# Kernel tuning notes

Hardware: AMD Instinct MI355X
Metric: run time of the kernel (lower is better)

Reference implementation:

```python
import jax, jax.numpy as jnp
import numpy as np

L, HID, NH, AD, FF = 6, 512, 8, 64, 2048
G, ST, NF, RA, RD = 8, 512, 25, 16, 20
T = G + 4 * ST  # 2056 tokens


def _ln(x, g, b, eps=1e-5):
    m = jnp.mean(x, axis=-1, keepdims=True)
    v = jnp.mean((x - m) ** 2, axis=-1, keepdims=True)
    return (x - m) * jax.lax.rsqrt(v + eps) * g + b


def _expand4(m, g):
    top = jnp.concatenate([m[:, :g, :g], jnp.repeat(m[:, :g, g:], 4, axis=2)], axis=2)
    bot = jnp.concatenate([jnp.repeat(m[:, g:, :g], 4, axis=1),
                           jnp.repeat(jnp.repeat(m[:, g:, g:], 4, axis=1), 4, axis=2)], axis=2)
    return jnp.concatenate([top, bot], axis=1)


def setup_inputs() -> dict:
    key = jax.random.key(0)
    ks = iter(jax.random.split(key, 48))
    n = lambda shape, s=0.02: (jax.random.normal(next(ks), shape, jnp.float32) * s)
    N = G + ST
    inp = {
        "obj_input": jax.random.normal(next(ks), (1, G, NF, 4), jnp.float32),
        "obj_scale": jax.random.normal(next(ks), (1, G, NF, 2), jnp.float32),
        "st_input0": jax.random.normal(next(ks), (1, ST, 10), jnp.float32),
        "rpe_a": jax.random.randint(next(ks), (1, N, N), 0, RA, jnp.int32),
        "rpe_d": jax.random.randint(next(ks), (1, N, N), 0, RD + 1, jnp.int32),
        "mask": jnp.zeros((1, N, N), jnp.float32),
        # projection heads
        "Wpg": n((4 * NF, HID)), "bpg": jnp.zeros((HID,)),
        "pg_g": jnp.ones((HID,)), "pg_b": jnp.zeros((HID,)),
        "Wps": n((2, HID)), "bps": jnp.zeros((HID,)),
        "ps_g": jnp.ones((HID,)), "ps_b": jnp.zeros((HID,)),
        # relative position embeddings
        "emb_a": n((RA, NH)), "emb_d": n((RD + 1, NH)),
        # stacked transformer layer params
        "Wq": n((L, HID, NH * AD)), "bq": jnp.zeros((L, NH * AD)),
        "Wk": n((L, HID, NH * AD)), "bk": jnp.zeros((L, NH * AD)),
        "Wv": n((L, HID, NH * AD)), "bv": jnp.zeros((L, NH * AD)),
        "Wo": n((L, NH * AD, HID)), "bo": jnp.zeros((L, HID)),
        "W1": n((L, HID, FF)), "b1": jnp.zeros((L, FF)),
        "W2": n((L, FF, HID)), "b2": jnp.zeros((L, HID)),
        "ln1_g": jnp.ones((L, HID)), "ln1_b": jnp.zeros((L, HID)),
        "ln2_g": jnp.ones((L, HID)), "ln2_b": jnp.zeros((L, HID)),
    }
    return inp


def reference(obj_input, obj_scale, st_input0, rpe_a, rpe_d, mask,
              Wpg, bpg, pg_g, pg_b, Wps, bps, ps_g, ps_b, emb_a, emb_d,
              Wq, bq, Wk, bk, Wv, bv, Wo, bo, W1, b1, W2, b2,
              ln1_g, ln1_b, ln2_g, ln2_b):
    g = obj_input.shape[1]
    # token embeddings: objects + strokes (4 points of 2 coords each)
    st = st_input0[:, :, :8].reshape(1, -1, 2)                       # [1, 4*ST, 2]
    obj_emb = jax.nn.leaky_relu(_ln(obj_input.reshape(1, g, -1) @ Wpg + bpg, pg_g, pg_b))
    st_emb = jax.nn.leaky_relu(_ln(st @ Wps + bps, ps_g, ps_b))
    x = jnp.concatenate([obj_emb, st_emb], axis=1)                   # [1, T, HID]
    t = x.shape[1]
    # relative-position bias: embed expanded angle/distance indices
    pos = emb_a[_expand4(rpe_a, g)] + emb_d[_expand4(rpe_d, g)]      # [1, T, T, NH]
    pos = jnp.transpose(pos, (0, 3, 1, 2))                           # [1, NH, T, T]
    msk = _expand4(mask, g)[:, None]                                 # [1, 1, T, T]
    inv_sqrt_d = np.float32(1.0 / np.sqrt(AD))
    for l in range(Wq.shape[0]):
        q = (x @ Wq[l] + bq[l]).reshape(1, t, NH, AD)
        k = (x @ Wk[l] + bk[l]).reshape(1, t, NH, AD)
        v = (x @ Wv[l] + bv[l]).reshape(1, t, NH, AD)
        # note: bias added BEFORE scaling, then mask (matches torch source)
        scores = (jnp.einsum('bqhd,bkhd->bhqk', q, k) + pos) * inv_sqrt_d + msk
        att = jax.nn.softmax(scores, axis=-1)
        o = jnp.einsum('bhqk,bkhd->bqhd', att, v).reshape(1, t, NH * AD)
        x = _ln(x + o @ Wo[l] + bo[l], ln1_g[l], ln1_b[l])
        h = jax.nn.leaky_relu(x @ W1[l] + b1[l])
        x = _ln(x + h @ W2[l] + b2[l], ln2_g[l], ln2_b[l])
    return x
```

## Files before the change

kernel.cpp:

```cpp
#include <hip/hip_runtime.h>
#include <math.h>

#define T_TOK 2056
#define TP 2176
#define TK 2112
#define HIDDEN 512
#define NHEAD 8
#define ADIM 64
#define FFDIM 2048
#define NLAYER 6
#define NORIG 520
#define NOBJ 8
#define NSPLIT 4

typedef float f32x4 __attribute__((ext_vector_type(4)));
typedef __attribute__((__ext_vector_type__(8))) __bf16 bf16x8;

__device__ __forceinline__ unsigned short f2bf(float f) {
  unsigned int u = __float_as_uint(f);
  u += 0x7FFFu + ((u >> 16) & 1u);
  return (unsigned short)(u >> 16);
}
__device__ __forceinline__ float bf2f(unsigned short u) {
  return __uint_as_float(((unsigned int)u) << 16);
}


__device__ inline float blockReduceSum(float v, float* sb) {
#pragma unroll
  for (int off = 32; off > 0; off >>= 1) v += __shfl_down(v, off, 64);
  int wid = threadIdx.x >> 6;
  __syncthreads();
  if ((threadIdx.x & 63) == 0) sb[wid] = v;
  __syncthreads();
  return sb[0] + sb[1] + sb[2] + sb[3];
}


__global__ __launch_bounds__(256) void embed_kernel(
    const float* __restrict__ obj, const float* __restrict__ st0,
    const float* __restrict__ Wpg, const float* __restrict__ bpg,
    const float* __restrict__ pg_g, const float* __restrict__ pg_b,
    const float* __restrict__ Wps, const float* __restrict__ bps,
    const float* __restrict__ ps_g, const float* __restrict__ ps_b,
    float* __restrict__ x, unsigned short* __restrict__ xb)
{
  __shared__ float sb[4];
  int t = blockIdx.x;
  int j0 = threadIdx.x, j1 = threadIdx.x + 256;
  float a0, a1;
  const float *g, *b;
  if (t < NOBJ) {
    a0 = bpg[j0]; a1 = bpg[j1];
    const float* in = obj + t * 100;
    for (int i = 0; i < 100; i++) {
      float w = in[i];
      a0 += w * Wpg[i * HIDDEN + j0];
      a1 += w * Wpg[i * HIDDEN + j1];
    }
    g = pg_g; b = pg_b;
  } else {
    int tt = t - NOBJ, s = tt >> 2, p = tt & 3;
    float c0 = st0[s * 10 + p * 2], c1 = st0[s * 10 + p * 2 + 1];
    a0 = bps[j0] + c0 * Wps[j0] + c1 * Wps[HIDDEN + j0];
    a1 = bps[j1] + c0 * Wps[j1] + c1 * Wps[HIDDEN + j1];
    g = ps_g; b = ps_b;
  }
  float s1 = blockReduceSum(a0 + a1, sb);
  float s2 = blockReduceSum(a0 * a0 + a1 * a1, sb);
  float m = s1 * (1.0f / HIDDEN);
  float var = s2 * (1.0f / HIDDEN) - m * m;
  float inv = rsqrtf(var + 1e-5f);
  float y0 = (a0 - m) * inv * g[j0] + b[j0];
  float y1 = (a1 - m) * inv * g[j1] + b[j1];
  y0 = y0 >= 0.f ? y0 : 0.01f * y0;
  y1 = y1 >= 0.f ? y1 : 0.01f * y1;
  x[t * HIDDEN + j0] = y0;
  x[t * HIDDEN + j1] = y1;
  xb[t * HIDDEN + j0] = f2bf(y0);
  xb[t * HIDDEN + j1] = f2bf(y1);
}

__global__ __launch_bounds__(256) void padzero(unsigned short* __restrict__ xb) {
  int i = blockIdx.x * 256 + threadIdx.x;
  if (i < (TP - T_TOK) * HIDDEN) xb[T_TOK * HIDDEN + i] = 0;
}


__global__ __launch_bounds__(256) void posbuild(
    const int* __restrict__ rpe_a, const int* __restrict__ rpe_d,
    const float* __restrict__ emb_a, const float* __restrict__ emb_d,
    const float* __restrict__ mask, unsigned short* __restrict__ posb)
{
  int i = blockIdx.x;
  for (int j = threadIdx.x; j < NORIG; j += 256) {
    int a = rpe_a[i * NORIG + j];
    int d = rpe_d[i * NORIG + j];
    float mk = mask[i * NORIG + j];
#pragma unroll
    for (int h = 0; h < NHEAD; h++) {
      float v = (emb_a[a * NHEAD + h] + emb_d[d * NHEAD + h]) * 0.125f + mk;
      posb[(h * NORIG + i) * NORIG + j] = f2bf(v);
    }
  }
}


__global__ __launch_bounds__(256) void wtrans(
    const float* __restrict__ Wq, const float* __restrict__ Wk, const float* __restrict__ Wv,
    const float* __restrict__ Wo, const float* __restrict__ W1, const float* __restrict__ W2,
    unsigned short* __restrict__ Wqkvt, unsigned short* __restrict__ Wot,
    unsigned short* __restrict__ W1t, unsigned short* __restrict__ W2t)
{
  __shared__ float t[64 * 65];
  int b = blockIdx.x;
  const float* src; unsigned short* dst; int N, K, tk, tn;
  if (b < 192) {
    int m = b >> 6, bb = b & 63;
    src = m == 0 ? Wq : m == 1 ? Wk : Wv;
    dst = Wqkvt + m * 512 * 512;
    K = 512; N = 512; tk = bb & 7; tn = bb >> 3;
  } else if (b < 256) {
    int bb = b - 192; src = Wo; dst = Wot; K = 512; N = 512; tk = bb & 7; tn = bb >> 3;
  } else if (b < 512) {
    int bb = b - 256; src = W1; dst = W1t; K = 512; N = 2048; tk = bb & 7; tn = bb >> 3;
  } else {
    int bb = b - 512; src = W2; dst = W2t; K = 2048; N = 512; tk = bb & 31; tn = bb >> 5;
  }
  int k0 = tk * 64, n0 = tn * 64;
  int tid = threadIdx.x;
  int r = tid >> 2, c0 = (tid & 3) * 16;
  const float* sp = src + (k0 + r) * N + n0 + c0;
#pragma unroll
  for (int q = 0; q < 4; q++) {
    float4 f = *(const float4*)(sp + q * 4);
    t[r * 65 + c0 + q * 4 + 0] = f.x;
    t[r * 65 + c0 + q * 4 + 1] = f.y;
    t[r * 65 + c0 + q * 4 + 2] = f.z;
    t[r * 65 + c0 + q * 4 + 3] = f.w;
  }
  __syncthreads();
  unsigned short vals[16];
#pragma unroll
  for (int j = 0; j < 16; j++) vals[j] = f2bf(t[(c0 + j) * 65 + r]);
  unsigned short* dp = dst + (n0 + r) * K + k0 + c0;
  *(int4*)dp = *(int4*)&vals[0];
  *(int4*)(dp + 8) = *(int4*)&vals[8];
}


__global__ __launch_bounds__(256) void gemm_bt(
    const unsigned short* __restrict__ A, int lda,
    const unsigned short* __restrict__ Bt, int ldb, int K, int mode,
    const float* __restrict__ b0, const float* __restrict__ b1, const float* __restrict__ b2,
    unsigned short* __restrict__ d0, unsigned short* __restrict__ d1, unsigned short* __restrict__ d2,
    float* __restrict__ df, int ldc)
{
  __shared__ unsigned short As[64 * 40];
  __shared__ unsigned short Bs[128 * 40];
  const int tid = threadIdx.x;
  const int lane = tid & 63, wave = tid >> 6;
  const int l15 = lane & 15, quad = lane >> 4;
  const int rowBase = blockIdx.y * 64, colBase = blockIdx.x * 128;
  const int mw = (wave & 1) * 32, nw = (wave >> 1) * 64;
  const int sr = tid >> 2, sc = (tid & 3) * 8;
  const int zz = blockIdx.z;
  const int kLen = K / gridDim.z;
  const int kb0 = zz * kLen;
  const unsigned short* Ag0 = A + (rowBase + sr) * lda + sc;
  const unsigned short* Bg0 = Bt + (colBase + sr) * ldb + sc;
  const unsigned short* Bg1 = Bg0 + 64 * ldb;
  f32x4 acc[2][4];
#pragma unroll
  for (int i = 0; i < 2; i++)
#pragma unroll
    for (int j = 0; j < 4; j++) acc[i][j] = (f32x4){0.f, 0.f, 0.f, 0.f};

  for (int kb = kb0; kb < kb0 + kLen; kb += 32) {
    int4 a0 = *(const int4*)(Ag0 + kb);
    int4 g0 = *(const int4*)(Bg0 + kb);
    int4 g1 = *(const int4*)(Bg1 + kb);
    __syncthreads();
    *(int4*)&As[sr * 40 + sc] = a0;
    *(int4*)&Bs[sr * 40 + sc] = g0;
    *(int4*)&Bs[(sr + 64) * 40 + sc] = g1;
    __syncthreads();
    bf16x8 af[2], bfr[4];
#pragma unroll
    for (int mt = 0; mt < 2; mt++)
      af[mt] = *(const bf16x8*)&As[(mw + mt * 16 + l15) * 40 + quad * 8];
#pragma unroll
    for (int nt = 0; nt < 4; nt++)
      bfr[nt] = *(const bf16x8*)&Bs[(nw + nt * 16 + l15) * 40 + quad * 8];
#pragma unroll
    for (int mt = 0; mt < 2; mt++)
#pragma unroll
      for (int nt = 0; nt < 4; nt++)
        acc[mt][nt] = __builtin_amdgcn_mfma_f32_16x16x32_bf16(af[mt], bfr[nt], acc[mt][nt], 0, 0, 0);
  }

  float* dfz = df + (size_t)zz * TP * ldc;
#pragma unroll
  for (int mt = 0; mt < 2; mt++) {
#pragma unroll
    for (int nt = 0; nt < 4; nt++) {
#pragma unroll
      for (int r = 0; r < 4; r++) {
        int row = rowBase + mw + mt * 16 + quad * 4 + r;
        int col = colBase + nw + nt * 16 + l15;
        float v = acc[mt][nt][r];
        if (mode == 0) {
          int seg = col >> 9, cc = col & 511;
          const float* bs = seg == 0 ? b0 : seg == 1 ? b1 : b2;
          unsigned short* dst = seg == 0 ? d0 : seg == 1 ? d1 : d2;
          int hd = cc >> 6, d = cc & 63;
          dst[(hd * TP + row) * 64 + d] = f2bf(v + bs[cc]);
        } else if (mode == 1) {
          dfz[row * ldc + col] = v;
        } else {
          float t = v + b0[col];
          t = t >= 0.f ? t : 0.01f * t;
          d0[row * ldc + col] = f2bf(t);
        }
      }
    }
  }
}


__global__ __launch_bounds__(256) void vt_trans(
    const unsigned short* __restrict__ vh, unsigned short* __restrict__ vt)
{
  __shared__ unsigned short t[64 * 72];
  int kt = blockIdx.x, h = blockIdx.y;
  int tid = threadIdx.x;
  int r0 = tid >> 3, cs = (tid & 7) * 8;
  const unsigned short* src = vh + (h * TP + kt * 64 + r0) * 64 + cs;
  *(int4*)&t[r0 * 72 + cs] = *(const int4*)src;
  *(int4*)&t[(r0 + 32) * 72 + cs] = *(const int4*)(src + 32 * 64);
  __syncthreads();
  int d = tid >> 2, c0 = (tid & 3) * 16;
  unsigned short vals[16];
#pragma unroll
  for (int j = 0; j < 16; j++) vals[j] = t[(c0 + j) * 72 + d];
  unsigned short* dst = vt + (h * 64 + d) * TK + kt * 64 + c0;
  *(int4*)dst = *(int4*)&vals[0];
  *(int4*)(dst + 8) = *(int4*)&vals[8];
}


__global__ __launch_bounds__(256) void flash_attn(
    const unsigned short* __restrict__ qh, const unsigned short* __restrict__ kh,
    const unsigned short* __restrict__ vt, const unsigned short* __restrict__ posb,
    float* __restrict__ Opart, float* __restrict__ ml)
{
  __shared__ unsigned short Ks[64 * 72];
  __shared__ unsigned short Vs[80 * 88];
  __shared__ unsigned short Ps[64 * 72];
  __shared__ float pt[24 * 24];
  const int tid = threadIdx.x;
  const int lane = tid & 63, wave = tid >> 6;
  const int l15 = lane & 15, quad = lane >> 4;
  const int qt = blockIdx.x, h = blockIdx.y, z = blockIdx.z;
  const int q0 = qt * 64;
  const int qrow = q0 + wave * 16 + l15;
  const unsigned short* qbp = qh + (h * TP + qrow) * 64;
  bf16x8 qf0 = *(const bf16x8*)(qbp + quad * 8);
  bf16x8 qf1 = *(const bf16x8*)(qbp + 32 + quad * 8);
  f32x4 O[5];
#pragma unroll
  for (int nt = 0; nt < 5; nt++) O[nt] = (f32x4){0.f, 0.f, 0.f, 0.f};
  for (int idx = tid; idx < 16 * 88; idx += 256) {
    int rr = idx / 88, cc = idx - rr * 88;
    Vs[(64 + rr) * 88 + cc] = (rr == 0) ? 0x3F80 : 0;
  }
  const int oq0 = q0 < 8 ? q0 : 8 + ((q0 - 8) >> 2);
  const int qe = min(q0 + 63, T_TOK - 1);
  const int nq = (qe < 8 ? qe : 8 + ((qe - 8) >> 2)) - oq0 + 1;
  int myq[4];
#pragma unroll
  for (int r = 0; r < 4; r++) {
    int qr = q0 + wave * 16 + quad * 4 + r;
    myq[r] = (qr < 8 ? qr : 8 + ((qr - 8) >> 2)) - oq0;
  }
  const int sr = tid >> 3, sc = (tid & 7) * 8;
  const unsigned short* kgb = kh + (h * TP + sr) * 64 + sc;
  const unsigned short* vgb = vt + (h * 64 + sr) * TK + sc;
  const int ptrow = tid >> 3, ptc0 = (tid & 7) * 3;

  const int kt0 = z * 9, kt1 = min(33, kt0 + 9);
  for (int kt = kt0; kt < kt1; kt++) {
    const int kb = kt * 64;
    int4 kv0 = *(const int4*)(kgb + kb * 64);
    int4 kv1 = *(const int4*)(kgb + (kb + 32) * 64);
    int4 vv0 = *(const int4*)(vgb + kb);
    int4 vv1 = *(const int4*)(vgb + 32 * TK + kb);
    const int ok0 = kb < 8 ? kb : 8 + ((kb - 8) >> 2);
    const int ke = min(kb + 63, T_TOK - 1);
    const int nk = (ke < 8 ? ke : 8 + ((ke - 8) >> 2)) - ok0 + 1;
    __syncthreads();
    *(int4*)&Ks[sr * 72 + sc] = kv0;
    *(int4*)&Ks[(sr + 32) * 72 + sc] = kv1;
    *(int4*)&Vs[sr * 88 + sc] = vv0;
    *(int4*)&Vs[(sr + 32) * 88 + sc] = vv1;
    if (ptrow < 24) {
      const unsigned short* prow = posb + (h * NORIG + oq0 + ptrow) * NORIG + ok0;
      bool rok = ptrow < nq;
#pragma unroll
      for (int c = 0; c < 3; c++) {
        int col = ptc0 + c;
        pt[ptrow * 24 + col] = (rok && col < nk) ? bf2f(prow[col]) : 0.f;
      }
    }
    __syncthreads();
    f32x4 S[4];
#pragma unroll
    for (int nt = 0; nt < 4; nt++) S[nt] = (f32x4){0.f, 0.f, 0.f, 0.f};
#pragma unroll
    for (int nt = 0; nt < 4; nt++) {
      bf16x8 kf0 = *(const bf16x8*)&Ks[(nt * 16 + l15) * 72 + quad * 8];
      bf16x8 kf1 = *(const bf16x8*)&Ks[(nt * 16 + l15) * 72 + 32 + quad * 8];
      S[nt] = __builtin_amdgcn_mfma_f32_16x16x32_bf16(qf0, kf0, S[nt], 0, 0, 0);
      S[nt] = __builtin_amdgcn_mfma_f32_16x16x32_bf16(qf1, kf1, S[nt], 0, 0, 0);
    }
    int okp[4], colv[4];
#pragma unroll
    for (int nt = 0; nt < 4; nt++) {
      int c = kb + nt * 16 + l15;
      colv[nt] = c;
      okp[nt] = (c < 8 ? c : 8 + ((c - 8) >> 2)) - ok0;
    }
#pragma unroll
    for (int r = 0; r < 4; r++) {
      int pr = wave * 16 + quad * 4 + r;
#pragma unroll
      for (int nt = 0; nt < 4; nt++) {
        float a = (colv[nt] < T_TOK)
                    ? fminf(S[nt][r] * 0.125f + pt[myq[r] * 24 + okp[nt]], 60.f)
                    : -1e30f;
        Ps[pr * 72 + nt * 16 + l15] = f2bf(__expf(a));
      }
    }
    __syncthreads();
    bf16x8 pa0 = *(const bf16x8*)&Ps[(wave * 16 + l15) * 72 + quad * 8];
    bf16x8 pa1 = *(const bf16x8*)&Ps[(wave * 16 + l15) * 72 + 32 + quad * 8];
#pragma unroll
    for (int nt = 0; nt < 5; nt++) {
      bf16x8 vb0 = *(const bf16x8*)&Vs[(nt * 16 + l15) * 88 + quad * 8];
      bf16x8 vb1 = *(const bf16x8*)&Vs[(nt * 16 + l15) * 88 + 32 + quad * 8];
      O[nt] = __builtin_amdgcn_mfma_f32_16x16x32_bf16(pa0, vb0, O[nt], 0, 0, 0);
      O[nt] = __builtin_amdgcn_mfma_f32_16x16x32_bf16(pa1, vb1, O[nt], 0, 0, 0);
    }
  }
#pragma unroll
  for (int r = 0; r < 4; r++) {
    float lsum = __shfl(O[4][r], lane & 48, 64);
    int orow = q0 + wave * 16 + quad * 4 + r;
    size_t base = ((size_t)(z * NHEAD + h) * TK + orow);
    if (l15 == 0) {
      ml[base * 2] = 0.f;
      ml[base * 2 + 1] = lsum;
    }
#pragma unroll
    for (int nt = 0; nt < 4; nt++)
      Opart[base * 64 + nt * 16 + l15] = O[nt][r];
  }
}


__global__ __launch_bounds__(256) void flash_merge(
    const float* __restrict__ Opart, const float* __restrict__ ml,
    unsigned short* __restrict__ ob)
{
  int idx = blockIdx.x * 256 + threadIdx.x;
  if (idx >= T_TOK * HIDDEN) return;
  int row = idx >> 9, c = idx & 511;
  int h = c >> 6, d = c & 63;
  float M = -1e30f;
  float mv[NSPLIT], lv[NSPLIT];
#pragma unroll
  for (int s = 0; s < NSPLIT; s++) {
    size_t base = ((size_t)(s * NHEAD + h) * TK + row);
    mv[s] = ml[base * 2];
    lv[s] = ml[base * 2 + 1];
    M = fmaxf(M, mv[s]);
  }
  float num = 0.f, den = 0.f;
#pragma unroll
  for (int s = 0; s < NSPLIT; s++) {
    float w = __expf(mv[s] - M);
    den += w * lv[s];
    num += w * Opart[((size_t)(s * NHEAD + h) * TK + row) * 64 + d];
  }
  ob[idx] = f2bf(num / den);
}


__global__ __launch_bounds__(256) void ln_residual4(
    float* __restrict__ x, const float* __restrict__ parts,
    const float* __restrict__ bias,
    const float* __restrict__ g, const float* __restrict__ b,
    unsigned short* __restrict__ xb)
{
  __shared__ float sb[4];
  int row = blockIdx.x;
  int j0 = threadIdx.x, j1 = threadIdx.x + 256;
  int base = row * HIDDEN;
  const size_t ss = (size_t)TP * HIDDEN;
  float v0 = x[base + j0] + bias[j0] + parts[base + j0] + parts[ss + base + j0]
           + parts[2 * ss + base + j0] + parts[3 * ss + base + j0];
  float v1 = x[base + j1] + bias[j1] + parts[base + j1] + parts[ss + base + j1]
           + parts[2 * ss + base + j1] + parts[3 * ss + base + j1];
  float s1 = blockReduceSum(v0 + v1, sb);
  float s2 = blockReduceSum(v0 * v0 + v1 * v1, sb);
  float m = s1 * (1.0f / HIDDEN);
  float var = s2 * (1.0f / HIDDEN) - m * m;
  float inv = rsqrtf(var + 1e-5f);
  float y0 = (v0 - m) * inv * g[j0] + b[j0];
  float y1 = (v1 - m) * inv * g[j1] + b[j1];
  x[base + j0] = y0;
  x[base + j1] = y1;
  xb[base + j0] = f2bf(y0);
  xb[base + j1] = f2bf(y1);
}

__global__ __launch_bounds__(256) void copy_out(
    const float4* __restrict__ src, float4* __restrict__ dst, int n4)
{
  int i = blockIdx.x * 256 + threadIdx.x;
  if (i < n4) dst[i] = src[i];
}


extern "C" void kernel_launch(void* const* d_in, const int* in_sizes, int n_in,
                              void* d_out, int out_size, void* d_ws, size_t ws_size,
                              hipStream_t stream) {
  const float* obj   = (const float*)d_in[0];
  const float* st0   = (const float*)d_in[2];
  const int*   rpe_a = (const int*)d_in[3];
  const int*   rpe_d = (const int*)d_in[4];
  const float* mask  = (const float*)d_in[5];
  const float* Wpg = (const float*)d_in[6];  const float* bpg = (const float*)d_in[7];
  const float* pg_g = (const float*)d_in[8]; const float* pg_b = (const float*)d_in[9];
  const float* Wps = (const float*)d_in[10]; const float* bps = (const float*)d_in[11];
  const float* ps_g = (const float*)d_in[12];const float* ps_b = (const float*)d_in[13];
  const float* emb_a = (const float*)d_in[14];
  const float* emb_d = (const float*)d_in[15];
  const float* Wq = (const float*)d_in[16]; const float* bq = (const float*)d_in[17];
  const float* Wk = (const float*)d_in[18]; const float* bk = (const float*)d_in[19];
  const float* Wv = (const float*)d_in[20]; const float* bv = (const float*)d_in[21];
  const float* Wo = (const float*)d_in[22]; const float* bo = (const float*)d_in[23];
  const float* W1 = (const float*)d_in[24]; const float* b1 = (const float*)d_in[25];
  const float* W2 = (const float*)d_in[26]; const float* b2 = (const float*)d_in[27];
  const float* ln1_g = (const float*)d_in[28]; const float* ln1_b = (const float*)d_in[29];
  const float* ln2_g = (const float*)d_in[30]; const float* ln2_b = (const float*)d_in[31];

  char* p = (char*)d_ws;
  auto alloc = [&](size_t bytes) { char* q = p; p += (bytes + 255) & ~(size_t)255; return q; };
  float*          x      = (float*)alloc((size_t)T_TOK * HIDDEN * 4);
  unsigned short* xb     = (unsigned short*)alloc((size_t)TP * HIDDEN * 2);
  char*           u1     = (char*)alloc((size_t)TP * FFDIM * 2);
  unsigned short* qhb    = (unsigned short*)u1;
  unsigned short* khb    = qhb + (size_t)NHEAD * TP * ADIM;
  unsigned short* vhb    = khb + (size_t)NHEAD * TP * ADIM;
  unsigned short* vtb    = vhb + (size_t)NHEAD * TP * ADIM;
  unsigned short* hb     = (unsigned short*)u1;
  unsigned short* ob     = (unsigned short*)alloc((size_t)TP * HIDDEN * 2);
  char*           u2     = (char*)alloc((size_t)NSPLIT * NHEAD * TK * ADIM * 4 + (size_t)NSPLIT * NHEAD * TK * 2 * 4);
  float*          Opart  = (float*)u2;
  float*          mlb    = Opart + (size_t)NSPLIT * NHEAD * TK * ADIM;
  float*          parts  = (float*)u2;
  unsigned short* posb   = (unsigned short*)alloc((size_t)NHEAD * NORIG * NORIG * 2);
  unsigned short* Wqkvt  = (unsigned short*)alloc((size_t)1536 * 512 * 2);
  unsigned short* Wot    = (unsigned short*)alloc((size_t)512 * 512 * 2);
  unsigned short* W1t    = (unsigned short*)alloc((size_t)2048 * 512 * 2);
  unsigned short* W2t    = (unsigned short*)alloc((size_t)512 * 2048 * 2);
  if ((size_t)(p - (char*)d_ws) > ws_size) return;

  float* out = (float*)d_out;

  embed_kernel<<<T_TOK, 256, 0, stream>>>(obj, st0, Wpg, bpg, pg_g, pg_b,
                                          Wps, bps, ps_g, ps_b, x, xb);
  padzero<<<((TP - T_TOK) * HIDDEN + 255) / 256, 256, 0, stream>>>(xb);
  posbuild<<<NORIG, 256, 0, stream>>>(rpe_a, rpe_d, emb_a, emb_d, mask, posb);

  for (int l = 0; l < NLAYER; l++) {
    wtrans<<<768, 256, 0, stream>>>(
        Wq + l * 512 * 512, Wk + l * 512 * 512, Wv + l * 512 * 512,
        Wo + l * 512 * 512, W1 + l * 512 * 2048, W2 + l * 2048 * 512,
        Wqkvt, Wot, W1t, W2t);
    gemm_bt<<<dim3(12, 34, 1), 256, 0, stream>>>(
        xb, HIDDEN, Wqkvt, HIDDEN, HIDDEN, 0,
        bq + l * 512, bk + l * 512, bv + l * 512, qhb, khb, vhb, nullptr, 0);
    vt_trans<<<dim3(33, 8), 256, 0, stream>>>(vhb, vtb);
    flash_attn<<<dim3(33, 8, NSPLIT), 256, 0, stream>>>(
        qhb, khb, vtb, posb, Opart, mlb);
    flash_merge<<<(T_TOK * HIDDEN + 255) / 256, 256, 0, stream>>>(Opart, mlb, ob);
    gemm_bt<<<dim3(4, 34, NSPLIT), 256, 0, stream>>>(
        ob, HIDDEN, Wot, HIDDEN, HIDDEN, 1,
        nullptr, nullptr, nullptr, nullptr, nullptr, nullptr, parts, HIDDEN);
    ln_residual4<<<T_TOK, 256, 0, stream>>>(x, parts, bo + l * 512,
                                            ln1_g + l * 512, ln1_b + l * 512, xb);
    gemm_bt<<<dim3(16, 34, 1), 256, 0, stream>>>(
        xb, HIDDEN, W1t, HIDDEN, HIDDEN, 2,
        b1 + l * 2048, nullptr, nullptr, hb, nullptr, nullptr, nullptr, FFDIM);
    gemm_bt<<<dim3(4, 34, NSPLIT), 256, 0, stream>>>(
        hb, FFDIM, W2t, FFDIM, FFDIM, 1,
        nullptr, nullptr, nullptr, nullptr, nullptr, nullptr, parts, HIDDEN);
    ln_residual4<<<T_TOK, 256, 0, stream>>>(x, parts, b2 + l * 512,
                                            ln2_g + l * 512, ln2_b + l * 512, xb);
  }

  int n4 = T_TOK * HIDDEN / 4;
  copy_out<<<(n4 + 255) / 256, 256, 0, stream>>>((const float4*)x, (float4*)out, n4);
}
```

Before: 1.004 ms.

## Double-buffer GEMM, prefetch flash tiles, use exp2 with prescaled Q, hoist weight transposes

The GEMM main loop now uses double-buffered LDS with register prefetch of the next K slice, which removes one barrier per iteration. The attention kernel splits keys 8 ways in an interleaved order and prefetches the next K/V/pos tile. It folds the 1/sqrt(d) scale and log2(e) into Q and the position bias so exp2 can be used, stores partial outputs as bf16, and drops one barrier. The merge becomes a plain sum, because no running max is kept. Weight transposes for all layers are done once up front when workspace allows, which adds memory use and relies on the clamp at 86 to avoid overflow.

```diff
diff --git a/kernel.cpp b/kernel.cpp
--- a/kernel.cpp
+++ b/kernel.cpp
@@ -12,9 +12,16 @@
 #define NORIG 520
 #define NOBJ 8
 #define NSPLIT 4
+#define FSPLIT 8
 
 typedef float f32x4 __attribute__((ext_vector_type(4)));
 typedef __attribute__((__ext_vector_type__(8))) __bf16 bf16x8;
+
+#if __has_builtin(__builtin_amdgcn_exp2f)
+#define EXP2(x) __builtin_amdgcn_exp2f(x)
+#else
+#define EXP2(x) exp2f(x)
+#endif
 
 __device__ __forceinline__ unsigned short f2bf(float f) {
   unsigned int u = __float_as_uint(f);
@@ -99,7 +106,7 @@
     float mk = mask[i * NORIG + j];
 #pragma unroll
     for (int h = 0; h < NHEAD; h++) {
-      float v = (emb_a[a * NHEAD + h] + emb_d[d * NHEAD + h]) * 0.125f + mk;
+      float v = ((emb_a[a * NHEAD + h] + emb_d[d * NHEAD + h]) * 0.125f + mk) * 1.44269504f;
       posb[(h * NORIG + i) * NORIG + j] = f2bf(v);
     }
   }
@@ -156,8 +163,8 @@
     unsigned short* __restrict__ d0, unsigned short* __restrict__ d1, unsigned short* __restrict__ d2,
     float* __restrict__ df, int ldc)
 {
-  __shared__ unsigned short As[64 * 40];
-  __shared__ unsigned short Bs[128 * 40];
+  __shared__ unsigned short As[2][64 * 40];
+  __shared__ unsigned short Bs[2][128 * 40];
   const int tid = threadIdx.x;
   const int lane = tid & 63, wave = tid >> 6;
   const int l15 = lane & 15, quad = lane >> 4;
@@ -167,6 +174,7 @@
   const int zz = blockIdx.z;
   const int kLen = K / gridDim.z;
   const int kb0 = zz * kLen;
+  const int nIter = kLen >> 5;
   const unsigned short* Ag0 = A + (rowBase + sr) * lda + sc;
   const unsigned short* Bg0 = Bt + (colBase + sr) * ldb + sc;
   const unsigned short* Bg1 = Bg0 + 64 * ldb;
@@ -176,27 +184,40 @@
 #pragma unroll
     for (int j = 0; j < 4; j++) acc[i][j] = (f32x4){0.f, 0.f, 0.f, 0.f};
 
-  for (int kb = kb0; kb < kb0 + kLen; kb += 32) {
-    int4 a0 = *(const int4*)(Ag0 + kb);
-    int4 g0 = *(const int4*)(Bg0 + kb);
-    int4 g1 = *(const int4*)(Bg1 + kb);
+  int4 a0 = *(const int4*)(Ag0 + kb0);
+  int4 g0 = *(const int4*)(Bg0 + kb0);
+  int4 g1 = *(const int4*)(Bg1 + kb0);
+  *(int4*)&As[0][sr * 40 + sc] = a0;
+  *(int4*)&Bs[0][sr * 40 + sc] = g0;
+  *(int4*)&Bs[0][(sr + 64) * 40 + sc] = g1;
+
+  for (int it = 0; it < nIter; ++it) {
     __syncthreads();
-    *(int4*)&As[sr * 40 + sc] = a0;
-    *(int4*)&Bs[sr * 40 + sc] = g0;
-    *(int4*)&Bs[(sr + 64) * 40 + sc] = g1;
-    __syncthreads();
+    const int cur = it & 1, nxt = cur ^ 1;
+    const bool more = (it + 1) < nIter;
+    if (more) {
+      int kb = kb0 + (it + 1) * 32;
+      a0 = *(const int4*)(Ag0 + kb);
+      g0 = *(const int4*)(Bg0 + kb);
+      g1 = *(const int4*)(Bg1 + kb);
+    }
     bf16x8 af[2], bfr[4];
 #pragma unroll
     for (int mt = 0; mt < 2; mt++)
-      af[mt] = *(const bf16x8*)&As[(mw + mt * 16 + l15) * 40 + quad * 8];
+      af[mt] = *(const bf16x8*)&As[cur][(mw + mt * 16 + l15) * 40 + quad * 8];
 #pragma unroll
     for (int nt = 0; nt < 4; nt++)
-      bfr[nt] = *(const bf16x8*)&Bs[(nw + nt * 16 + l15) * 40 + quad * 8];
+      bfr[nt] = *(const bf16x8*)&Bs[cur][(nw + nt * 16 + l15) * 40 + quad * 8];
 #pragma unroll
     for (int mt = 0; mt < 2; mt++)
 #pragma unroll
       for (int nt = 0; nt < 4; nt++)
         acc[mt][nt] = __builtin_amdgcn_mfma_f32_16x16x32_bf16(af[mt], bfr[nt], acc[mt][nt], 0, 0, 0);
+    if (more) {
+      *(int4*)&As[nxt][sr * 40 + sc] = a0;
+      *(int4*)&Bs[nxt][sr * 40 + sc] = g0;
+      *(int4*)&Bs[nxt][(sr + 64) * 40 + sc] = g1;
+    }
   }
 
   float* dfz = df + (size_t)zz * TP * ldc;
@@ -214,7 +235,9 @@
           const float* bs = seg == 0 ? b0 : seg == 1 ? b1 : b2;
           unsigned short* dst = seg == 0 ? d0 : seg == 1 ? d1 : d2;
           int hd = cc >> 6, d = cc & 63;
-          dst[(hd * TP + row) * 64 + d] = f2bf(v + bs[cc]);
+          float t = v + bs[cc];
+          if (seg == 0) t *= 0.180336880111f;
+          dst[(hd * TP + row) * 64 + d] = f2bf(t);
         } else if (mode == 1) {
           dfz[row * ldc + col] = v;
         } else {
@@ -252,7 +275,7 @@
 __global__ __launch_bounds__(256) void flash_attn(
     const unsigned short* __restrict__ qh, const unsigned short* __restrict__ kh,
     const unsigned short* __restrict__ vt, const unsigned short* __restrict__ posb,
-    float* __restrict__ Opart, float* __restrict__ ml)
+    unsigned short* __restrict__ Opart, float* __restrict__ lbuf)
 {
   __shared__ unsigned short Ks[64 * 72];
   __shared__ unsigned short Vs[80 * 88];
@@ -287,32 +310,53 @@
   const unsigned short* kgb = kh + (h * TP + sr) * 64 + sc;
   const unsigned short* vgb = vt + (h * 64 + sr) * TK + sc;
   const int ptrow = tid >> 3, ptc0 = (tid & 7) * 3;
-
-  const int kt0 = z * 9, kt1 = min(33, kt0 + 9);
-  for (int kt = kt0; kt < kt1; kt++) {
-    const int kb = kt * 64;
-    int4 kv0 = *(const int4*)(kgb + kb * 64);
-    int4 kv1 = *(const int4*)(kgb + (kb + 32) * 64);
-    int4 vv0 = *(const int4*)(vgb + kb);
-    int4 vv1 = *(const int4*)(vgb + 32 * TK + kb);
-    const int ok0 = kb < 8 ? kb : 8 + ((kb - 8) >> 2);
-    const int ke = min(kb + 63, T_TOK - 1);
-    const int nk = (ke < 8 ? ke : 8 + ((ke - 8) >> 2)) - ok0 + 1;
+  const bool prok = (ptrow < 24) && (ptrow < nq);
+
+  const int nT = (33 - z + FSPLIT - 1) / FSPLIT;
+  int kb = z * 64;
+  int4 kv0 = *(const int4*)(kgb + kb * 64);
+  int4 kv1 = *(const int4*)(kgb + (kb + 32) * 64);
+  int4 vv0 = *(const int4*)(vgb + kb);
+  int4 vv1 = *(const int4*)(vgb + 32 * TK + kb);
+  float ppf0, ppf1, ppf2;
+  {
+    int ok0n = kb < 8 ? kb : 8 + ((kb - 8) >> 2);
+    int ken = min(kb + 63, T_TOK - 1);
+    int nkn = (ken < 8 ? ken : 8 + ((ken - 8) >> 2)) - ok0n + 1;
+    const unsigned short* prow = posb + (h * NORIG + oq0 + ptrow) * NORIG + ok0n;
+    ppf0 = (prok && ptc0 + 0 < nkn) ? bf2f(prow[ptc0 + 0]) : 0.f;
+    ppf1 = (prok && ptc0 + 1 < nkn) ? bf2f(prow[ptc0 + 1]) : 0.f;
+    ppf2 = (prok && ptc0 + 2 < nkn) ? bf2f(prow[ptc0 + 2]) : 0.f;
+  }
+
+  for (int i = 0; i < nT; ++i) {
+    const int kbCur = kb;
+    const int ok0c = kbCur < 8 ? kbCur : 8 + ((kbCur - 8) >> 2);
     __syncthreads();
     *(int4*)&Ks[sr * 72 + sc] = kv0;
     *(int4*)&Ks[(sr + 32) * 72 + sc] = kv1;
     *(int4*)&Vs[sr * 88 + sc] = vv0;
     *(int4*)&Vs[(sr + 32) * 88 + sc] = vv1;
     if (ptrow < 24) {
-      const unsigned short* prow = posb + (h * NORIG + oq0 + ptrow) * NORIG + ok0;
-      bool rok = ptrow < nq;
-#pragma unroll
-      for (int c = 0; c < 3; c++) {
-        int col = ptc0 + c;
-        pt[ptrow * 24 + col] = (rok && col < nk) ? bf2f(prow[col]) : 0.f;
-      }
+      pt[ptrow * 24 + ptc0 + 0] = ppf0;
+      pt[ptrow * 24 + ptc0 + 1] = ppf1;
+      pt[ptrow * 24 + ptc0 + 2] = ppf2;
     }
     __syncthreads();
+    kb += FSPLIT * 64;
+    if (i + 1 < nT) {
+      kv0 = *(const int4*)(kgb + kb * 64);
+      kv1 = *(const int4*)(kgb + (kb + 32) * 64);
+      vv0 = *(const int4*)(vgb + kb);
+      vv1 = *(const int4*)(vgb + 32 * TK + kb);
+      int ok0n = kb < 8 ? kb : 8 + ((kb - 8) >> 2);
+      int ken = min(kb + 63, T_TOK - 1);
+      int nkn = (ken < 8 ? ken : 8 + ((ken - 8) >> 2)) - ok0n + 1;
+      const unsigned short* prow = posb + (h * NORIG + oq0 + ptrow) * NORIG + ok0n;
+      ppf0 = (prok && ptc0 + 0 < nkn) ? bf2f(prow[ptc0 + 0]) : 0.f;
+      ppf1 = (prok && ptc0 + 1 < nkn) ? bf2f(prow[ptc0 + 1]) : 0.f;
+      ppf2 = (prok && ptc0 + 2 < nkn) ? bf2f(prow[ptc0 + 2]) : 0.f;
+    }
     f32x4 S[4];
 #pragma unroll
     for (int nt = 0; nt < 4; nt++) S[nt] = (f32x4){0.f, 0.f, 0.f, 0.f};
@@ -323,25 +367,22 @@
       S[nt] = __builtin_amdgcn_mfma_f32_16x16x32_bf16(qf0, kf0, S[nt], 0, 0, 0);
       S[nt] = __builtin_amdgcn_mfma_f32_16x16x32_bf16(qf1, kf1, S[nt], 0, 0, 0);
     }
-    int okp[4], colv[4];
+    int okp[4]; bool cval[4];
 #pragma unroll
     for (int nt = 0; nt < 4; nt++) {
-      int c = kb + nt * 16 + l15;
-      colv[nt] = c;
-      okp[nt] = (c < 8 ? c : 8 + ((c - 8) >> 2)) - ok0;
+      int c = kbCur + nt * 16 + l15;
+      cval[nt] = c < T_TOK;
+      okp[nt] = (c < 8 ? c : 8 + ((c - 8) >> 2)) - ok0c;
     }
 #pragma unroll
     for (int r = 0; r < 4; r++) {
       int pr = wave * 16 + quad * 4 + r;
 #pragma unroll
       for (int nt = 0; nt < 4; nt++) {
-        float a = (colv[nt] < T_TOK)
-                    ? fminf(S[nt][r] * 0.125f + pt[myq[r] * 24 + okp[nt]], 60.f)
-                    : -1e30f;
-        Ps[pr * 72 + nt * 16 + l15] = f2bf(__expf(a));
+        float a = cval[nt] ? fminf(S[nt][r] + pt[myq[r] * 24 + okp[nt]], 86.f) : -1e30f;
+        Ps[pr * 72 + nt * 16 + l15] = f2bf(EXP2(a));
       }
     }
-    __syncthreads();
     bf16x8 pa0 = *(const bf16x8*)&Ps[(wave * 16 + l15) * 72 + quad * 8];
     bf16x8 pa1 = *(const bf16x8*)&Ps[(wave * 16 + l15) * 72 + 32 + quad * 8];
 #pragma unroll
@@ -354,43 +395,30 @@
   }
 #pragma unroll
   for (int r = 0; r < 4; r++) {
-    float lsum = __shfl(O[4][r], lane & 48, 64);
     int orow = q0 + wave * 16 + quad * 4 + r;
     size_t base = ((size_t)(z * NHEAD + h) * TK + orow);
-    if (l15 == 0) {
-      ml[base * 2] = 0.f;
-      ml[base * 2 + 1] = lsum;
-    }
+    if (l15 == 0) lbuf[base] = O[4][r];
 #pragma unroll
     for (int nt = 0; nt < 4; nt++)
-      Opart[base * 64 + nt * 16 + l15] = O[nt][r];
+      Opart[base * 64 + nt * 16 + l15] = f2bf(O[nt][r]);
   }
 }
 
 
 __global__ __launch_bounds__(256) void flash_merge(
-    const float* __restrict__ Opart, const float* __restrict__ ml,
+    const unsigned short* __restrict__ Opart, const float* __restrict__ lbuf,
     unsigned short* __restrict__ ob)
 {
   int idx = blockIdx.x * 256 + threadIdx.x;
   if (idx >= T_TOK * HIDDEN) return;
   int row = idx >> 9, c = idx & 511;
   int h = c >> 6, d = c & 63;
-  float M = -1e30f;
-  float mv[NSPLIT], lv[NSPLIT];
-#pragma unroll
-  for (int s = 0; s < NSPLIT; s++) {
+  float num = 0.f, den = 0.f;
+#pragma unroll
+  for (int s = 0; s < FSPLIT; s++) {
     size_t base = ((size_t)(s * NHEAD + h) * TK + row);
-    mv[s] = ml[base * 2];
-    lv[s] = ml[base * 2 + 1];
-    M = fmaxf(M, mv[s]);
-  }
-  float num = 0.f, den = 0.f;
-#pragma unroll
-  for (int s = 0; s < NSPLIT; s++) {
-    float w = __expf(mv[s] - M);
-    den += w * lv[s];
-    num += w * Opart[((size_t)(s * NHEAD + h) * TK + row) * 64 + d];
+    den += lbuf[base];
+    num += bf2f(Opart[base * 64 + d]);
   }
   ob[idx] = f2bf(num / den);
 }
@@ -466,16 +494,26 @@
   unsigned short* vtb    = vhb + (size_t)NHEAD * TP * ADIM;
   unsigned short* hb     = (unsigned short*)u1;
   unsigned short* ob     = (unsigned short*)alloc((size_t)TP * HIDDEN * 2);
-  char*           u2     = (char*)alloc((size_t)NSPLIT * NHEAD * TK * ADIM * 4 + (size_t)NSPLIT * NHEAD * TK * 2 * 4);
-  float*          Opart  = (float*)u2;
-  float*          mlb    = Opart + (size_t)NSPLIT * NHEAD * TK * ADIM;
+  size_t opartB = (size_t)FSPLIT * NHEAD * TK * ADIM * 2;
+  size_t partsB = (size_t)NSPLIT * TP * HIDDEN * 4;
+  size_t u2B = opartB + (size_t)FSPLIT * NHEAD * TK * 4;
+  if (partsB > u2B) u2B = partsB;
+  char*           u2     = (char*)alloc(u2B);
+  unsigned short* Opart  = (unsigned short*)u2;
+  float*          lbb    = (float*)(u2 + opartB);
   float*          parts  = (float*)u2;
   unsigned short* posb   = (unsigned short*)alloc((size_t)NHEAD * NORIG * NORIG * 2);
-  unsigned short* Wqkvt  = (unsigned short*)alloc((size_t)1536 * 512 * 2);
-  unsigned short* Wot    = (unsigned short*)alloc((size_t)512 * 512 * 2);
-  unsigned short* W1t    = (unsigned short*)alloc((size_t)2048 * 512 * 2);
-  unsigned short* W2t    = (unsigned short*)alloc((size_t)512 * 2048 * 2);
+  size_t perLayerW = ((size_t)1536 * 512 + 512 * 512 + 2048 * 512 + 512 * 2048) * 2;
+  size_t baseUsed = (size_t)(p - (char*)d_ws);
+  bool hoist = (baseUsed + 6 * perLayerW + 2048) <= ws_size;
+  int nWsets = hoist ? 6 : 1;
+  unsigned short* Wsets = (unsigned short*)alloc(perLayerW * nWsets);
   if ((size_t)(p - (char*)d_ws) > ws_size) return;
+
+  auto wq_t = [&](int l) { return Wsets + (hoist ? l : 0) * (perLayerW / 2); };
+  auto wo_t = [&](int l) { return wq_t(l) + (size_t)1536 * 512; };
+  auto w1_t = [&](int l) { return wo_t(l) + (size_t)512 * 512; };
+  auto w2_t = [&](int l) { return w1_t(l) + (size_t)2048 * 512; };
 
   float* out = (float*)d_out;
 
@@ -483,29 +521,38 @@
                                           Wps, bps, ps_g, ps_b, x, xb);
   padzero<<<((TP - T_TOK) * HIDDEN + 255) / 256, 256, 0, stream>>>(xb);
   posbuild<<<NORIG, 256, 0, stream>>>(rpe_a, rpe_d, emb_a, emb_d, mask, posb);
+  if (hoist) {
+    for (int l = 0; l < NLAYER; l++)
+      wtrans<<<768, 256, 0, stream>>>(
+          Wq + l * 512 * 512, Wk + l * 512 * 512, Wv + l * 512 * 512,
+          Wo + l * 512 * 512, W1 + l * 512 * 2048, W2 + l * 2048 * 512,
+          wq_t(l), wo_t(l), w1_t(l), w2_t(l));
+  }
 
   for (int l = 0; l < NLAYER; l++) {
-    wtrans<<<768, 256, 0, stream>>>(
-        Wq + l * 512 * 512, Wk + l * 512 * 512, Wv + l * 512 * 512,
-        Wo + l * 512 * 512, W1 + l * 512 * 2048, W2 + l * 2048 * 512,
-        Wqkvt, Wot, W1t, W2t);
+    if (!hoist) {
+      wtrans<<<768, 256, 0, stream>>>(
+          Wq + l * 512 * 512, Wk + l * 512 * 512, Wv + l * 512 * 512,
+          Wo + l * 512 * 512, W1 + l * 512 * 2048, W2 + l * 2048 * 512,
+          wq_t(l), wo_t(l), w1_t(l), w2_t(l));
+    }
     gemm_bt<<<dim3(12, 34, 1), 256, 0, stream>>>(
-        xb, HIDDEN, Wqkvt, HIDDEN, HIDDEN, 0,
+        xb, HIDDEN, wq_t(l), HIDDEN, HIDDEN, 0,
         bq + l * 512, bk + l * 512, bv + l * 512, qhb, khb, vhb, nullptr, 0);
     vt_trans<<<dim3(33, 8), 256, 0, stream>>>(vhb, vtb);
-    flash_attn<<<dim3(33, 8, NSPLIT), 256, 0, stream>>>(
-        qhb, khb, vtb, posb, Opart, mlb);
-    flash_merge<<<(T_TOK * HIDDEN + 255) / 256, 256, 0, stream>>>(Opart, mlb, ob);
+    flash_attn<<<dim3(33, 8, FSPLIT), 256, 0, stream>>>(
+        qhb, khb, vtb, posb, Opart, lbb);
+    flash_merge<<<(T_TOK * HIDDEN + 255) / 256, 256, 0, stream>>>(Opart, lbb, ob);
     gemm_bt<<<dim3(4, 34, NSPLIT), 256, 0, stream>>>(
-        ob, HIDDEN, Wot, HIDDEN, HIDDEN, 1,
+        ob, HIDDEN, wo_t(l), HIDDEN, HIDDEN, 1,
         nullptr, nullptr, nullptr, nullptr, nullptr, nullptr, parts, HIDDEN);
     ln_residual4<<<T_TOK, 256, 0, stream>>>(x, parts, bo + l * 512,
                                             ln1_g + l * 512, ln1_b + l * 512, xb);
     gemm_bt<<<dim3(16, 34, 1), 256, 0, stream>>>(
-        xb, HIDDEN, W1t, HIDDEN, HIDDEN, 2,
+        xb, HIDDEN, w1_t(l), HIDDEN, HIDDEN, 2,
         b1 + l * 2048, nullptr, nullptr, hb, nullptr, nullptr, nullptr, FFDIM);
     gemm_bt<<<dim3(4, 34, NSPLIT), 256, 0, stream>>>(
-        hb, FFDIM, W2t, FFDIM, FFDIM, 1,
+        hb, FFDIM, w2_t(l), FFDIM, FFDIM, 1,
         nullptr, nullptr, nullptr, nullptr, nullptr, nullptr, parts, HIDDEN);
     ln_residual4<<<T_TOK, 256, 0, stream>>>(x, parts, b2 + l * 512,
                                             ln2_g + l * 512, ln2_b + l * 512, xb);
```

Result: faster. 960.8 us (-4.3%).
